# Kernel tuning notes

Measured on AMD Instinct MI355X. Metric: run time of the kernel, lower is better.

Reference implementation:

```python
import jax, jax.numpy as jnp
import numpy as np

B, C_IN, H, W = 32, 128, 64, 64
C_OUT, KH, KW = 256, 3, 3


def setup_inputs() -> dict:
    key = jax.random.key(0)
    k1, k2, k3 = jax.random.split(key, 3)
    inputs = jax.random.normal(k1, (B, C_IN, H, W), dtype=jnp.float32)
    weights = jax.random.normal(k2, (C_OUT, C_IN, KH, KW), dtype=jnp.float32) * 0.05
    bias = jax.random.normal(k3, (C_OUT, 1), dtype=jnp.float32)
    return {"inputs": inputs, "weights": weights, "bias": bias}


def reference(inputs, weights, bias):
    # Direct 2D valid convolution, stride 1, padding 0 (module default).
    # output[b,o,i,j] = sum_{c,u,v} inputs[b,c,i+u,j+v] * weights[o,c,u,v] + bias[o]
    out = jax.lax.conv_general_dilated(
        inputs, weights,
        window_strides=(1, 1),
        padding="VALID",
        dimension_numbers=("NCHW", "OIHW", "NCHW"),
    )
    # bias has shape (C_out, 1); broadcast per output channel
    return out + bias.reshape(1, -1, 1, 1)
```

## Files before the change

### kernel.cpp

```cpp
#include <hip/hip_runtime.h>
#include <hip/hip_bf16.h>
#include <stdint.h>

#define BB   32
#define CIN  128
#define HH   64
#define WW   64
#define COUT 256
#define OHH  62
#define OWW  62
#define PIX_PER_B (OHH*OWW)
#define NPIX (BB*PIX_PER_B)
#define KTOT (9*CIN)
#define NKT  36
#define SLOT 24576

typedef __bf16 bf16x8 __attribute__((ext_vector_type(8)));
typedef float  f32x4  __attribute__((ext_vector_type(4)));
typedef uint16_t u16x8 __attribute__((ext_vector_type(8)));

__device__ __forceinline__ uint16_t f2bf(float f) {
    uint32_t u = __float_as_uint(f);
    uint32_t r = (u + 0x7FFFu + ((u >> 16) & 1u)) >> 16;
    return (uint16_t)r;
}

__device__ __forceinline__ void gload_lds16(const void* g, void* l) {
    __builtin_amdgcn_global_load_lds(
        (const __attribute__((address_space(1))) uint32_t*)g,
        (__attribute__((address_space(3))) uint32_t*)l, 16, 0, 0);
}

__global__ void __launch_bounds__(256) to_nhwc(const float* __restrict__ in,
                                               uint16_t* __restrict__ out) {
    int slab = blockIdx.x;
    int b = slab >> 6, h = slab & 63;
    int w  = threadIdx.x & 63;
    int cp = threadIdx.x >> 6;
    const float* src = in + (((size_t)b * CIN) * HH + h) * WW + w;
    uint16_t* dst = out + ((size_t)slab * WW + w) * CIN;
    #pragma unroll
    for (int it = 0; it < 4; ++it) {
        int c0 = cp * 32 + it * 8;
        u16x8 v;
        #pragma unroll
        for (int j = 0; j < 8; ++j) v[j] = f2bf(src[(c0 + j) * (HH * WW)]);
        *reinterpret_cast<u16x8*>(dst + c0) = v;
    }
}

__global__ void __launch_bounds__(256) pack_w(const float* __restrict__ w,
                                              uint16_t* __restrict__ out) {
    int idx = blockIdx.x * 256 + threadIdx.x;
    int o = idx / KTOT;
    int k = idx - o * KTOT;
    int uv = k >> 7, c = k & 127;
    out[idx] = f2bf(w[(o * CIN + c) * 9 + uv]);
}

__global__ void __launch_bounds__(512, 4) conv_k32(
        const uint16_t* __restrict__ Xg,
        const uint16_t* __restrict__ Wg,
        const float*    __restrict__ bias,
        float*          __restrict__ out)
{
    __shared__ char lds[2 * SLOT + 1024];
    int* pbase = (int*)(lds + 2 * SLOT);
    int* obase = pbase + 128;

    const int tid  = threadIdx.x;
    const int lane = tid & 63;
    const int wid  = tid >> 6;

    int bid = blockIdx.x;
    int xcd = bid & 7, lid = bid >> 3;
    int nt  = (xcd == 0 ? lid : 121 + (xcd - 1) * 120 + lid);

    if (tid < 128) {
        int n   = nt * 128 + tid;
        int b   = n / PIX_PER_B;
        int rem = n - b * PIX_PER_B;
        int oh  = rem / OWW;
        int ow  = rem - oh * OWW;
        pbase[tid] = ((b * 64 + oh) * 64 + ow) * 128;
        obase[tid] = b * (COUT * PIX_PER_B) + rem;
    }
    __syncthreads();

    const int cs   = (((tid & 3) ^ ((tid >> 3) & 3)) << 4);
    const int ldst = tid * 16;
    const char* aptr0 = (const char*)Wg + (tid >> 2) * (KTOT * 2) + cs;
    const char* aptr1 = (const char*)Wg + (128 + (tid >> 2)) * (KTOT * 2) + cs;
    const char* xptr  = (const char*)Xg + pbase[tid >> 2] * 2 + cs;

    const int wm = wid >> 1, wn = wid & 1;
    int aro[4], xro[4];
    #pragma unroll
    for (int mi = 0; mi < 4; ++mi) {
        int row = wm * 64 + mi * 16 + (lane & 15);
        aro[mi] = row * 64 + ((((lane >> 4) ^ ((row >> 1) & 3))) << 4);
    }
    #pragma unroll
    for (int nj = 0; nj < 4; ++nj) {
        int row = wn * 64 + nj * 16 + (lane & 15);
        xro[nj] = 16384 + row * 64 + ((((lane >> 4) ^ ((row >> 1) & 3))) << 4);
    }

    f32x4 acc[4][4] = {};

    auto stage = [&](int t, char* dst) {
        int uvv = t >> 2;
        int u   = (uvv * 11) >> 5;
        int v   = uvv - u * 3;
        int xo  = (u << 14) | (v << 8) | ((t & 3) << 6);
        gload_lds16(aptr0 + t * 64, dst + ldst);
        gload_lds16(aptr1 + t * 64, dst + 8192 + ldst);
        gload_lds16(xptr + xo, dst + 16384 + ldst);
    };

#define PH(T, S, STG, VMC, BAR) do {                                           \
    if (STG) stage((T) + 1, lds + (1 - (S)) * SLOT);                           \
    const char* _s = lds + (S) * SLOT;                                         \
    bf16x8 af[4], xf[4];                                                       \
    _Pragma("unroll") for (int mi = 0; mi < 4; ++mi)                           \
        af[mi] = *reinterpret_cast<const bf16x8*>(_s + aro[mi]);               \
    _Pragma("unroll") for (int nj = 0; nj < 4; ++nj)                           \
        xf[nj] = *reinterpret_cast<const bf16x8*>(_s + xro[nj]);               \
    __builtin_amdgcn_s_setprio(1);                                             \
    _Pragma("unroll") for (int mi = 0; mi < 4; ++mi)                           \
      _Pragma("unroll") for (int nj = 0; nj < 4; ++nj)                         \
        acc[mi][nj] = __builtin_amdgcn_mfma_f32_16x16x32_bf16(                 \
            af[mi], xf[nj], acc[mi][nj], 0, 0, 0);                             \
    __builtin_amdgcn_s_setprio(0);                                             \
    if (VMC) asm volatile("s_waitcnt vmcnt(0)" ::: "memory");                  \
    if (BAR) __builtin_amdgcn_s_barrier();                                     \
} while (0)

    stage(0, lds);
    asm volatile("s_waitcnt vmcnt(0)" ::: "memory");
    __builtin_amdgcn_s_barrier();

    for (int i = 0; i < 17; ++i) {
        PH(2 * i + 0, 0, 1, 1, 1);
        PH(2 * i + 1, 1, 1, 1, 1);
    }
    PH(34, 0, 1, 1, 1);
    PH(35, 1, 0, 0, 0);
#undef PH

    #pragma unroll
    for (int mi = 0; mi < 4; ++mi) {
        int o = wm * 64 + mi * 16 + ((lane >> 4) << 2);
        #pragma unroll
        for (int reg = 0; reg < 4; ++reg) {
            float bv = bias[o + reg];
            #pragma unroll
            for (int nj = 0; nj < 4; ++nj) {
                int pl = wn * 64 + nj * 16 + (lane & 15);
                out[obase[pl] + (o + reg) * PIX_PER_B] = acc[mi][nj][reg] + bv;
            }
        }
    }
}

__global__ void __launch_bounds__(256) conv_naive(const float* __restrict__ in,
                                                  const float* __restrict__ w,
                                                  const float* __restrict__ bias,
                                                  float* __restrict__ out) {
    long idx = (long)blockIdx.x * 256 + threadIdx.x;
    int t = (int)idx;
    int ow = t % OWW; t /= OWW;
    int oh = t % OHH; t /= OHH;
    int o  = t % COUT;
    int b  = t / COUT;
    float s = bias[o];
    for (int c = 0; c < CIN; ++c)
        for (int u = 0; u < 3; ++u)
            for (int v = 0; v < 3; ++v)
                s += in[((b * CIN + c) * HH + oh + u) * WW + ow + v] *
                     w[((o * CIN + c) * 3 + u) * 3 + v];
    out[idx] = s;
}

extern "C" void kernel_launch(void* const* d_in, const int* in_sizes, int n_in,
                              void* d_out, int out_size, void* d_ws, size_t ws_size,
                              hipStream_t stream) {
    const float* in   = (const float*)d_in[0];
    const float* wt   = (const float*)d_in[1];
    const float* bias = (const float*)d_in[2];
    float* out = (float*)d_out;

    const size_t xg_elems = (size_t)BB * HH * WW * CIN;
    const size_t wg_elems = (size_t)COUT * KTOT;
    const size_t need = (xg_elems + wg_elems) * sizeof(uint16_t);

    if (ws_size < need) {
        long total = (long)BB * COUT * OHH * OWW;
        conv_naive<<<(int)((total + 255) / 256), 256, 0, stream>>>(in, wt, bias, out);
        return;
    }

    uint16_t* Xg = (uint16_t*)d_ws;
    uint16_t* Wg = Xg + xg_elems;

    to_nhwc<<<BB * HH, 256, 0, stream>>>(in, Xg);
    pack_w<<<(COUT * KTOT) / 256, 256, 0, stream>>>(wt, Wg);
    conv_k32<<<NPIX / 128, 512, 0, stream>>>(Xg, Wg, bias, out);
}
```

Before: 109.5 us.

## Load activation fragments directly into registers and split output channels across blocks

The conv kernel now uses 256-thread blocks that each cover 128 output channels by 128 pixels, launching twice as many blocks. Activation (X) fragments are read straight from global memory into registers with one-step-ahead prefetching, instead of being staged through LDS. Only the weights are double-buffered in LDS, one 3x3 tap (uv) per stage, so there are 9 barriers instead of 36. The trade-off is that X is no longer shared between waves through LDS, which means more global/L2 traffic and exposed load latency, in return for less LDS pressure and fewer syncs.

```diff
diff --git a/kernel.cpp b/kernel.cpp
--- a/kernel.cpp
+++ b/kernel.cpp
@@ -12,8 +12,7 @@
 #define PIX_PER_B (OHH*OWW)
 #define NPIX (BB*PIX_PER_B)
 #define KTOT (9*CIN)
-#define NKT  36
-#define SLOT 24576
+#define WROW (KTOT*2)
 
 typedef __bf16 bf16x8 __attribute__((ext_vector_type(8)));
 typedef float  f32x4  __attribute__((ext_vector_type(4)));
@@ -58,14 +57,14 @@
     out[idx] = f2bf(w[(o * CIN + c) * 9 + uv]);
 }
 
-__global__ void __launch_bounds__(512, 4) conv_k32(
+__global__ void __launch_bounds__(256, 3) conv_xreg(
         const uint16_t* __restrict__ Xg,
         const uint16_t* __restrict__ Wg,
         const float*    __restrict__ bias,
         float*          __restrict__ out)
 {
-    __shared__ char lds[2 * SLOT + 1024];
-    int* pbase = (int*)(lds + 2 * SLOT);
+    __shared__ char lds[2 * 32768 + 1024];
+    int* pbase = (int*)(lds + 65536);
     int* obase = pbase + 128;
 
     const int tid  = threadIdx.x;
@@ -74,10 +73,12 @@
 
     int bid = blockIdx.x;
     int xcd = bid & 7, lid = bid >> 3;
-    int nt  = (xcd == 0 ? lid : 121 + (xcd - 1) * 120 + lid);
+    int swz = (xcd < 2 ? xcd * 241 : 482 + (xcd - 2) * 240) + lid;
+    const int mt = swz & 1;
+    const int pt = swz >> 1;
 
     if (tid < 128) {
-        int n   = nt * 128 + tid;
+        int n   = pt * 128 + tid;
         int b   = n / PIX_PER_B;
         int rem = n - b * PIX_PER_B;
         int oh  = rem / OWW;
@@ -89,68 +90,83 @@
 
     const int cs   = (((tid & 3) ^ ((tid >> 3) & 3)) << 4);
     const int ldst = tid * 16;
-    const char* aptr0 = (const char*)Wg + (tid >> 2) * (KTOT * 2) + cs;
-    const char* aptr1 = (const char*)Wg + (128 + (tid >> 2)) * (KTOT * 2) + cs;
-    const char* xptr  = (const char*)Xg + pbase[tid >> 2] * 2 + cs;
+    const char* aL = (const char*)Wg + (mt * 128 + (tid >> 2)) * WROW + cs;
+    const char* aH = aL + 64 * WROW;
+
+    auto stageA = [&](int uv, char* slot) {
+        int off = uv * 256;
+        #pragma unroll
+        for (int j = 0; j < 8; ++j) {
+            const char* src = ((j & 1) ? aH : aL) + off + (j >> 1) * 64;
+            gload_lds16(src, slot + j * 4096 + ldst);
+        }
+    };
 
     const int wm = wid >> 1, wn = wid & 1;
-    int aro[4], xro[4];
+    int aoff[4];
     #pragma unroll
     for (int mi = 0; mi < 4; ++mi) {
         int row = wm * 64 + mi * 16 + (lane & 15);
-        aro[mi] = row * 64 + ((((lane >> 4) ^ ((row >> 1) & 3))) << 4);
-    }
+        aoff[mi] = row * 64 + ((((lane >> 4) ^ ((row >> 1) & 3))) << 4);
+    }
+
+    const char* xb[4];
     #pragma unroll
     for (int nj = 0; nj < 4; ++nj) {
-        int row = wn * 64 + nj * 16 + (lane & 15);
-        xro[nj] = 16384 + row * 64 + ((((lane >> 4) ^ ((row >> 1) & 3))) << 4);
+        int p = wn * 64 + nj * 16 + (lane & 15);
+        xb[nj] = (const char*)Xg + (size_t)pbase[p] * 2 + ((lane >> 4) << 4);
     }
 
     f32x4 acc[4][4] = {};
-
-    auto stage = [&](int t, char* dst) {
-        int uvv = t >> 2;
-        int u   = (uvv * 11) >> 5;
-        int v   = uvv - u * 3;
-        int xo  = (u << 14) | (v << 8) | ((t & 3) << 6);
-        gload_lds16(aptr0 + t * 64, dst + ldst);
-        gload_lds16(aptr1 + t * 64, dst + 8192 + ldst);
-        gload_lds16(xptr + xo, dst + 16384 + ldst);
-    };
-
-#define PH(T, S, STG, VMC, BAR) do {                                           \
-    if (STG) stage((T) + 1, lds + (1 - (S)) * SLOT);                           \
-    const char* _s = lds + (S) * SLOT;                                         \
-    bf16x8 af[4], xf[4];                                                       \
+    bf16x8 xfA[4], xfB[4];
+    char* s0 = lds;
+    char* s1 = lds + 32768;
+
+#define PHX(SLOTP, PH, XC, XN, DOPRE, PREOFF) do {                             \
+    if (DOPRE) { _Pragma("unroll") for (int nj = 0; nj < 4; ++nj)              \
+        XN[nj] = *reinterpret_cast<const bf16x8*>(xb[nj] + (PREOFF)); }        \
+    bf16x8 af[4];                                                              \
     _Pragma("unroll") for (int mi = 0; mi < 4; ++mi)                           \
-        af[mi] = *reinterpret_cast<const bf16x8*>(_s + aro[mi]);               \
-    _Pragma("unroll") for (int nj = 0; nj < 4; ++nj)                           \
-        xf[nj] = *reinterpret_cast<const bf16x8*>(_s + xro[nj]);               \
+        af[mi] = *reinterpret_cast<const bf16x8*>(                             \
+            (SLOTP) + (PH) * 8192 + aoff[mi]);                                 \
     __builtin_amdgcn_s_setprio(1);                                             \
     _Pragma("unroll") for (int mi = 0; mi < 4; ++mi)                           \
       _Pragma("unroll") for (int nj = 0; nj < 4; ++nj)                         \
         acc[mi][nj] = __builtin_amdgcn_mfma_f32_16x16x32_bf16(                 \
-            af[mi], xf[nj], acc[mi][nj], 0, 0, 0);                             \
+            af[mi], XC[nj], acc[mi][nj], 0, 0, 0);                             \
     __builtin_amdgcn_s_setprio(0);                                             \
-    if (VMC) asm volatile("s_waitcnt vmcnt(0)" ::: "memory");                  \
-    if (BAR) __builtin_amdgcn_s_barrier();                                     \
 } while (0)
 
-    stage(0, lds);
+    stageA(0, s0);
+    #pragma unroll
+    for (int nj = 0; nj < 4; ++nj)
+        xfA[nj] = *reinterpret_cast<const bf16x8*>(xb[nj]);
     asm volatile("s_waitcnt vmcnt(0)" ::: "memory");
     __builtin_amdgcn_s_barrier();
 
-    for (int i = 0; i < 17; ++i) {
-        PH(2 * i + 0, 0, 1, 1, 1);
-        PH(2 * i + 1, 1, 1, 1, 1);
-    }
-    PH(34, 0, 1, 1, 1);
-    PH(35, 1, 0, 0, 0);
-#undef PH
+    #pragma unroll
+    for (int uv = 0; uv < 9; ++uv) {
+        char* sc = (uv & 1) ? s1 : s0;
+        char* sn = (uv & 1) ? s0 : s1;
+        const int u  = uv / 3, v = uv - (uv / 3) * 3;
+        const int xo = (u << 14) | (v << 8);
+        const int un = uv + 1;
+        const int nxo = ((un / 3) << 14) | ((un - (un / 3) * 3) << 8);
+        if (uv < 8) stageA(uv + 1, sn);
+        PHX(sc, 0, xfA, xfB, 1, xo + 64);
+        PHX(sc, 1, xfB, xfA, 1, xo + 128);
+        PHX(sc, 2, xfA, xfB, 1, xo + 192);
+        PHX(sc, 3, xfB, xfA, (uv < 8), nxo);
+        if (uv < 8) {
+            asm volatile("s_waitcnt vmcnt(0)" ::: "memory");
+            __builtin_amdgcn_s_barrier();
+        }
+    }
+#undef PHX
 
     #pragma unroll
     for (int mi = 0; mi < 4; ++mi) {
-        int o = wm * 64 + mi * 16 + ((lane >> 4) << 2);
+        int o = mt * 128 + wm * 64 + mi * 16 + ((lane >> 4) << 2);
         #pragma unroll
         for (int reg = 0; reg < 4; ++reg) {
             float bv = bias[o + reg];
@@ -205,5 +221,5 @@
 
     to_nhwc<<<BB * HH, 256, 0, stream>>>(in, Xg);
     pack_w<<<(COUT * KTOT) / 256, 256, 0, stream>>>(wt, Wg);
-    conv_k32<<<NPIX / 128, 512, 0, stream>>>(Xg, Wg, bias, out);
-}
+    conv_xreg<<<2 * (NPIX / 128), 256, 0, stream>>>(Xg, Wg, bias, out);
+}
```

New measurement: 183.0 us. 1.67x slower.
